# Kernel optimization log

Measured on AMD Instinct MI355X. Metric: run time of the kernel, lower is better.

## Reference

```python
import jax, jax.numpy as jnp
import numpy as np

L, B, H, Y, C = 256, 256, 256, 32, 16  # seq len, batch, hidden, y_size, spline channels (u_size+1)


def setup_inputs() -> dict:
    key = jax.random.key(0)
    ks = jax.random.split(key, 10)
    # times: uniform grid 0..L-1 (torchcde default spline parameterization), shape (L,B,1)
    ts = jnp.broadcast_to(jnp.arange(L, dtype=jnp.float32)[:, None, None], (L, B, 1))
    us = jax.random.normal(ks[0], (L, B, C - 1), dtype=jnp.float32)
    h0 = 0.1 * jax.random.normal(ks[1], (B, H), dtype=jnp.float32)
    s = 1.0 / np.sqrt(H)
    # NCDEFunc: Linear(H,H) -> relu -> Linear(H, H*C) -> tanh -> view(B,H,C)
    W1 = jax.random.uniform(ks[2], (H, H), jnp.float32, -s, s)
    b1 = jax.random.uniform(ks[3], (H,), jnp.float32, -s, s)
    W2 = jax.random.uniform(ks[4], (H, H * C), jnp.float32, -s, s)
    b2 = jax.random.uniform(ks[5], (H * C,), jnp.float32, -s, s)
    # decoder MLP(H, 2H, Y, 1): Linear(H,2H) -> tanh -> Linear(2H,Y)
    dW1 = jax.random.uniform(ks[6], (H, 2 * H), jnp.float32, -s, s)
    db1 = jax.random.uniform(ks[7], (2 * H,), jnp.float32, -s, s)
    s2 = 1.0 / np.sqrt(2 * H)
    dW2 = jax.random.uniform(ks[8], (2 * H, Y), jnp.float32, -s2, s2)
    db2 = jax.random.uniform(ks[9], (Y,), jnp.float32, -s2, s2)
    return dict(ts=ts, us=us, h0=h0, W1=W1, b1=b1, W2=W2, b2=b2,
                dW1=dW1, db1=db1, dW2=dW2, db2=db2)


def reference(ts, us, h0, W1, b1, W2, b2, dW1, db1, dW2, db2):
    # permute to batch-first and build control path x: (B, L, C)
    xb = jnp.concatenate([jnp.transpose(ts, (1, 0, 2)), jnp.transpose(us, (1, 0, 2))], axis=2)
    # hermite cubic with backward differences on unit grid (torchcde default t=arange):
    # node derivative d_i = x_i - x_{i-1} (delta=1); d_0 = d_1
    diffs = xb[:, 1:] - xb[:, :-1]                      # (B, L-1, C)
    dnode = jnp.concatenate([diffs[:, :1], diffs], axis=1)  # (B, L, C)
    t = ts[:, 0, 0]  # (L,) -- cdeint t grid = ts.squeeze(-1)[0,:] after permute

    def dXdt(s_):
        # derivative of the hermite cubic spline at scalar time s_ (unit knot spacing)
        idx = jnp.clip(jnp.floor(s_).astype(jnp.int32), 0, L - 2)
        tau = s_ - idx.astype(s_.dtype)
        xi, xip = xb[:, idx], xb[:, idx + 1]            # (B, C)
        di, dip = dnode[:, idx], dnode[:, idx + 1]
        h00p = 6.0 * tau * tau - 6.0 * tau              # h01' = -h00'
        h10p = 3.0 * tau * tau - 4.0 * tau + 1.0
        h11p = 3.0 * tau * tau - 2.0 * tau
        return h00p * (xi - xip) + h10p * di + h11p * dip  # (B, C)

    def vf(z):
        # NCDEFunc: z (B,H) -> matrix (B,H,C)
        hid = jax.nn.relu(z @ W1 + b1)
        return jnp.tanh(hid @ W2 + b2).reshape(B, H, C)

    def step(z, inp):
        s_, dt_ = inp
        dz = jnp.einsum('bhc,bc->bh', vf(z), dXdt(s_))  # f(z) @ dX/dt
        zn = z + dt_ * dz                               # Euler update on grid t
        return zn, zn

    _, zs = jax.lax.scan(step, h0, (t[:-1], t[1:] - t[:-1]))
    z_seq = jnp.concatenate([h0[None], zs], axis=0)     # (L, B, H): cdeint output at all t
    # decoder then permute(1,0,2) -> already time-major here: (L, B, Y)
    return jnp.tanh(z_seq @ dW1 + db1) @ dW2 + db2
```

## Files before the change

kernel.cpp:

```cpp
#include <hip/hip_runtime.h>
#include <math.h>

#define LL 256
#define BB 256
#define HH 256
#define CC 16
#define YY 32
#define HC (HH*CC)
#define NSTEP (LL-1)
#define NBG 32
#define BGB 8
#define HCH 32
#define TPB 1024
#define NJS 8

typedef __attribute__((ext_vector_type(4))) float f32x4;

__device__ __forceinline__ float fast_tanh(float x) {
    float e = __expf(2.0f * x);
    return 1.0f - 2.0f / (e + 1.0f);
}

__device__ __forceinline__ float ld_coh(const float* p) {
    return __hip_atomic_load(p, __ATOMIC_RELAXED, __HIP_MEMORY_SCOPE_AGENT);
}
__device__ __forceinline__ float2 ld_coh2(const float* p) {
    union { unsigned long long u; float2 f; } cv;
    cv.u = __hip_atomic_load((const unsigned long long*)p,
                             __ATOMIC_RELAXED, __HIP_MEMORY_SCOPE_AGENT);
    return cv.f;
}
__device__ __forceinline__ void st_coh(float* p, float v) {
    __hip_atomic_store(p, v, __ATOMIC_RELAXED, __HIP_MEMORY_SCOPE_AGENT);
}

__device__ __forceinline__ void bg_barrier(unsigned* cnt, unsigned target) {
    __syncthreads();
    if (threadIdx.x == 0) {
        __hip_atomic_fetch_add(cnt, 1u, __ATOMIC_RELAXED, __HIP_MEMORY_SCOPE_AGENT);
        while (__hip_atomic_load(cnt, __ATOMIC_RELAXED, __HIP_MEMORY_SCOPE_AGENT) < target)
            __builtin_amdgcn_s_sleep(1);
    }
    __syncthreads();
}

__global__ void __launch_bounds__(TPB, 4)
k_scan(const float* __restrict__ us, const float* __restrict__ W1,
       const float* __restrict__ b1, const float* __restrict__ W2,
       const float* __restrict__ b2, float* __restrict__ zs,
       float* __restrict__ hidG, unsigned* __restrict__ barG) {
    __shared__ float smem[NJS * BGB * 512 + 2048 + 2048 + 512 + 128 + 32];
    float* psum    = smem;
    float* pa      = smem;
    float* z_loc   = smem + NJS * BGB * 512;
    float* hid_loc = z_loc + BGB * HH;
    float* b2s     = hid_loc + BGB * HH;
    float* dvs     = b2s + 512;
    float* b1s     = dvs + 128;

    const int bg = blockIdx.x >> 3;
    const int hc = blockIdx.x & 7;
    const int t  = threadIdx.x;
    const int b0 = bg * BGB;
    const int h0 = hc * HCH;
    const int n0 = h0 * CC;

    const int ajc = t >> 5;
    const int ah  = t & 31;
    float w1r[8];
    #pragma unroll
    for (int r = 0; r < 8; r++)
        w1r[r] = W1[(size_t)(ajc * 8 + r) * HH + h0 + ah];
    for (int i = t; i < 512; i += TPB) b2s[i] = b2[n0 + i];
    if (t < HCH) b1s[t] = b1[h0 + t];
    __syncthreads();

    unsigned* cnt = barG + (size_t)bg * 64;

    const int sb  = t >> 7;
    const int sj2 = (t & 127) << 1;
    const int jsp = t >> 7;
    const int ct  = (t & 127) << 2;
    const int col = t & 511;
    const int bh  = (t >> 9) << 2;

    for (int k = 0; k < NSTEP; k++) {
        const size_t zk = (size_t)k * (BB * HH);

        {
            float2 v = ld_coh2(&zs[zk + (size_t)(b0 + sb) * HH + sj2]);
            *(float2*)&z_loc[sb * HH + sj2] = v;
        }
        if (t < BGB * CC) {
            int b = t >> 4, c = t & 15;
            int kk = (k < 1) ? 1 : k;
            float v = 1.0f;
            if (c > 0)
                v = us[((size_t)kk * BB + b0 + b) * (CC - 1) + c - 1]
                  - us[((size_t)(kk - 1) * BB + b0 + b) * (CC - 1) + c - 1];
            dvs[b * CC + c] = v;
        }
        __syncthreads();

        {
            float acc[BGB];
            #pragma unroll
            for (int b = 0; b < BGB; b++) acc[b] = 0.f;
            #pragma unroll
            for (int r2 = 0; r2 < 2; r2++) {
                #pragma unroll
                for (int b = 0; b < BGB; b++) {
                    float4 zv = *(const float4*)&z_loc[b * HH + ajc * 8 + r2 * 4];
                    acc[b] += zv.x * w1r[r2 * 4 + 0] + zv.y * w1r[r2 * 4 + 1]
                            + zv.z * w1r[r2 * 4 + 2] + zv.w * w1r[r2 * 4 + 3];
                }
            }
            #pragma unroll
            for (int b = 0; b < BGB; b++)
                pa[ajc * 256 + b * HCH + ah] = acc[b];
        }
        __syncthreads();
        if (t < BGB * HCH) {
            float s = b1s[t & 31];
            #pragma unroll
            for (int q = 0; q < 32; q++) s += pa[q * 256 + t];
            st_coh(&hidG[(size_t)(b0 + (t >> 5)) * HH + h0 + (t & 31)],
                   fmaxf(s, 0.f));
        }
        bg_barrier(cnt, 8u * (2u * (unsigned)k + 1u));

        {
            float2 v = ld_coh2(&hidG[(size_t)(b0 + sb) * HH + sj2]);
            *(float2*)&hid_loc[sb * HH + sj2] = v;
        }
        __syncthreads();

        {
            f32x4 acc[BGB];
            #pragma unroll
            for (int b = 0; b < BGB; b++) acc[b] = (f32x4){0.f, 0.f, 0.f, 0.f};
            const int jb = jsp * 32;
            const float* w2p = &W2[(size_t)jb * HC + n0 + ct];
            #pragma unroll 2
            for (int jq = 0; jq < 32; jq += 4) {
                f32x4 w0 = *(const f32x4*)&w2p[(size_t)(jq + 0) * HC];
                f32x4 w1 = *(const f32x4*)&w2p[(size_t)(jq + 1) * HC];
                f32x4 w2v = *(const f32x4*)&w2p[(size_t)(jq + 2) * HC];
                f32x4 w3 = *(const f32x4*)&w2p[(size_t)(jq + 3) * HC];
                #pragma unroll
                for (int b = 0; b < BGB; b++) {
                    f32x4 h4 = *(const f32x4*)&hid_loc[b * HH + jb + jq];
                    acc[b] = h4.x * w0  + acc[b];
                    acc[b] = h4.y * w1  + acc[b];
                    acc[b] = h4.z * w2v + acc[b];
                    acc[b] = h4.w * w3  + acc[b];
                }
            }
            #pragma unroll
            for (int b = 0; b < BGB; b++)
                *(f32x4*)&psum[((jsp * BGB + b) << 9) + ct] = acc[b];
        }
        __syncthreads();

        {
            #pragma unroll
            for (int q = 0; q < 4; q++) {
                int b = bh + q;
                float g = b2s[col];
                #pragma unroll
                for (int s = 0; s < NJS; s++)
                    g += psum[((s * BGB + b) << 9) + col];
                float v = fast_tanh(g) * dvs[b * CC + (col & 15)];
                v += __shfl_xor(v, 1);
                v += __shfl_xor(v, 2);
                v += __shfl_xor(v, 4);
                v += __shfl_xor(v, 8);
                if ((col & 15) == 0) {
                    int hl = col >> 4;
                    st_coh(&zs[zk + (size_t)(BB * HH) + (size_t)(b0 + b) * HH + h0 + hl],
                           z_loc[b * HH + h0 + hl] + v);
                }
            }
        }
        bg_barrier(cnt, 8u * (2u * (unsigned)k + 2u));
    }
}

__global__ void k_out(const float* __restrict__ zseq, const float* __restrict__ dW1,
                      const float* __restrict__ db1, const float* __restrict__ dW2,
                      const float* __restrict__ db2, float* __restrict__ out) {
    __shared__ float zt[16][HH];
    __shared__ float act[16][2 * HH];
    int r0 = blockIdx.x * 16;
    int t  = threadIdx.x;
    {
        const float4* src = (const float4*)(zseq + (size_t)r0 * HH);
        float4* dst = (float4*)&zt[0][0];
        for (int i = t; i < 1024; i += 256) dst[i] = src[i];
    }
    __syncthreads();
    {
        int c0  = (t & 127) * 4;
        int rr0 = (t >> 7) * 8;
        float a[8][4];
        #pragma unroll
        for (int i = 0; i < 8; i++)
            #pragma unroll
            for (int q = 0; q < 4; q++) a[i][q] = 0.f;
        for (int j = 0; j < HH; j++) {
            float4 w = *(const float4*)&dW1[(size_t)j * 2 * HH + c0];
            #pragma unroll
            for (int i = 0; i < 8; i++) {
                float zv = zt[rr0 + i][j];
                a[i][0] += zv * w.x; a[i][1] += zv * w.y;
                a[i][2] += zv * w.z; a[i][3] += zv * w.w;
            }
        }
        float4 bias = *(const float4*)&db1[c0];
        #pragma unroll
        for (int i = 0; i < 8; i++) {
            act[rr0 + i][c0 + 0] = fast_tanh(a[i][0] + bias.x);
            act[rr0 + i][c0 + 1] = fast_tanh(a[i][1] + bias.y);
            act[rr0 + i][c0 + 2] = fast_tanh(a[i][2] + bias.z);
            act[rr0 + i][c0 + 3] = fast_tanh(a[i][3] + bias.w);
        }
    }
    __syncthreads();
    {
        int rl = t >> 4;
        int y2 = t & 15;
        float o0 = 0.f, o1 = 0.f;
        #pragma unroll 4
        for (int j = 0; j < 2 * HH; j++) {
            float av = act[rl][j];
            float2 w = *(const float2*)&dW2[(size_t)j * YY + y2 * 2];
            o0 += av * w.x; o1 += av * w.y;
        }
        float2 bias = *(const float2*)&db2[y2 * 2];
        out[(size_t)(r0 + rl) * YY + y2 * 2]     = o0 + bias.x;
        out[(size_t)(r0 + rl) * YY + y2 * 2 + 1] = o1 + bias.y;
    }
}

extern "C" void kernel_launch(void* const* d_in, const int* in_sizes, int n_in,
                              void* d_out, int out_size, void* d_ws, size_t ws_size,
                              hipStream_t stream) {
    const float* us  = (const float*)d_in[1];
    const float* h0  = (const float*)d_in[2];
    const float* W1  = (const float*)d_in[3];
    const float* b1  = (const float*)d_in[4];
    const float* W2  = (const float*)d_in[5];
    const float* b2  = (const float*)d_in[6];
    const float* dW1 = (const float*)d_in[7];
    const float* db1 = (const float*)d_in[8];
    const float* dW2 = (const float*)d_in[9];
    const float* db2 = (const float*)d_in[10];
    float* out = (float*)d_out;

    float* zs   = (float*)d_ws;
    float* hidG = zs + (size_t)LL * BB * HH;
    unsigned* barG = (unsigned*)(hidG + (size_t)BB * HH);

    hipMemcpyAsync(zs, h0, (size_t)BB * HH * sizeof(float),
                   hipMemcpyDeviceToDevice, stream);
    hipMemsetAsync(barG, 0, NBG * 64 * sizeof(unsigned), stream);

    k_scan<<<NBG * 8, TPB, 0, stream>>>(us, W1, b1, W2, b2, zs, hidG, barG);
    k_out<<<LL * BB / 16, 256, 0, stream>>>(zs, dW1, db1, dW2, db2, out);
}
```

Measured before the change: 3.513 ms.

## Interleave two batch groups per block with split arrive/wait barriers

Each block now handles two 8-row batch groups (A and B) over a 16-wide hidden slice, instead of one batch group over a 32-wide slice, so 16 blocks cooperate per group pair. The grid barrier is split into separate arrive and wait calls, so one group's compute can overlap the other group's barrier latency. The intent is to hide the cross-block synchronisation cost of the sequential scan. In exchange, each block does less work per phase, W2 is streamed twice per step, and each barrier has more participants (16 instead of 8).

```diff
diff --git a/kernel.cpp b/kernel.cpp
--- a/kernel.cpp
+++ b/kernel.cpp
@@ -10,20 +10,18 @@
 #define NSTEP (LL-1)
 #define NBG 32
 #define BGB 8
-#define HCH 32
+#define NSIB 16
+#define COLS 256
 #define TPB 1024
 #define NJS 8
 
-typedef __attribute__((ext_vector_type(4))) float f32x4;
+typedef __attribute__((ext_vector_type(2))) float f32x2;
 
 __device__ __forceinline__ float fast_tanh(float x) {
     float e = __expf(2.0f * x);
     return 1.0f - 2.0f / (e + 1.0f);
 }
 
-__device__ __forceinline__ float ld_coh(const float* p) {
-    return __hip_atomic_load(p, __ATOMIC_RELAXED, __HIP_MEMORY_SCOPE_AGENT);
-}
 __device__ __forceinline__ float2 ld_coh2(const float* p) {
     union { unsigned long long u; float2 f; } cv;
     cv.u = __hip_atomic_load((const unsigned long long*)p,
@@ -34,13 +32,15 @@
     __hip_atomic_store(p, v, __ATOMIC_RELAXED, __HIP_MEMORY_SCOPE_AGENT);
 }
 
-__device__ __forceinline__ void bg_barrier(unsigned* cnt, unsigned target) {
-    __syncthreads();
-    if (threadIdx.x == 0) {
+__device__ __forceinline__ void bg_arrive(unsigned* cnt) {
+    __syncthreads();
+    if (threadIdx.x == 0)
         __hip_atomic_fetch_add(cnt, 1u, __ATOMIC_RELAXED, __HIP_MEMORY_SCOPE_AGENT);
+}
+__device__ __forceinline__ void bg_wait(unsigned* cnt, unsigned target) {
+    if (threadIdx.x == 0)
         while (__hip_atomic_load(cnt, __ATOMIC_RELAXED, __HIP_MEMORY_SCOPE_AGENT) < target)
             __builtin_amdgcn_s_sleep(1);
-    }
     __syncthreads();
 }
 
@@ -49,140 +49,165 @@
        const float* __restrict__ b1, const float* __restrict__ W2,
        const float* __restrict__ b2, float* __restrict__ zs,
        float* __restrict__ hidG, unsigned* __restrict__ barG) {
-    __shared__ float smem[NJS * BGB * 512 + 2048 + 2048 + 512 + 128 + 32];
-    float* psum    = smem;
-    float* pa      = smem;
-    float* z_loc   = smem + NJS * BGB * 512;
-    float* hid_loc = z_loc + BGB * HH;
-    float* b2s     = hid_loc + BGB * HH;
-    float* dvs     = b2s + 512;
-    float* b1s     = dvs + 128;
-
-    const int bg = blockIdx.x >> 3;
-    const int hc = blockIdx.x & 7;
-    const int t  = threadIdx.x;
-    const int b0 = bg * BGB;
-    const int h0 = hc * HCH;
-    const int n0 = h0 * CC;
-
-    const int ajc = t >> 5;
-    const int ah  = t & 31;
+    __shared__ __align__(16) float smem[23056];
+    float* psum = smem;
+    float* pa   = smem;
+    float* zA   = smem + 16384;
+    float* zB   = zA + 2048;
+    float* hidL = zB + 2048;
+    float* dvsA = hidL + 2048;
+    float* dvsB = dvsA + 128;
+    float* b2s  = dvsB + 128;
+    float* b1s  = b2s + 256;
+
+    const int bp  = blockIdx.x >> 4;
+    const int hc  = (blockIdx.x & 7) * 2 + ((blockIdx.x >> 3) & 1);
+    const int t   = threadIdx.x;
+    const int b0A = (bp * 2) * BGB;
+    const int b0B = (bp * 2 + 1) * BGB;
+    const int h0  = hc * 16;
+    const int n0  = h0 * CC;
+
+    const int ah   = t & 15;
+    const int ajc  = (t >> 4) & 31;
+    const int half = t >> 9;
     float w1r[8];
     #pragma unroll
     for (int r = 0; r < 8; r++)
         w1r[r] = W1[(size_t)(ajc * 8 + r) * HH + h0 + ah];
-    for (int i = t; i < 512; i += TPB) b2s[i] = b2[n0 + i];
-    if (t < HCH) b1s[t] = b1[h0 + t];
-    __syncthreads();
-
-    unsigned* cnt = barG + (size_t)bg * 64;
+    for (int i = t; i < COLS; i += TPB) b2s[i] = b2[n0 + i];
+    if (t < 16) b1s[t] = b1[h0 + t];
+    __syncthreads();
+
+    unsigned* cntA = barG + (size_t)(bp * 2) * 64;
+    unsigned* cntB = barG + (size_t)(bp * 2 + 1) * 64;
 
     const int sb  = t >> 7;
     const int sj2 = (t & 127) << 1;
     const int jsp = t >> 7;
-    const int ct  = (t & 127) << 2;
-    const int col = t & 511;
-    const int bh  = (t >> 9) << 2;
+    const int cp  = (t & 127) << 1;
+    const int col = t & 255;
+    const int bh  = (t >> 8) << 1;
 
     for (int k = 0; k < NSTEP; k++) {
         const size_t zk = (size_t)k * (BB * HH);
 
-        {
-            float2 v = ld_coh2(&zs[zk + (size_t)(b0 + sb) * HH + sj2]);
-            *(float2*)&z_loc[sb * HH + sj2] = v;
-        }
-        if (t < BGB * CC) {
-            int b = t >> 4, c = t & 15;
-            int kk = (k < 1) ? 1 : k;
-            float v = 1.0f;
-            if (c > 0)
-                v = us[((size_t)kk * BB + b0 + b) * (CC - 1) + c - 1]
-                  - us[((size_t)(kk - 1) * BB + b0 + b) * (CC - 1) + c - 1];
-            dvs[b * CC + c] = v;
-        }
-        __syncthreads();
-
-        {
-            float acc[BGB];
-            #pragma unroll
-            for (int b = 0; b < BGB; b++) acc[b] = 0.f;
-            #pragma unroll
-            for (int r2 = 0; r2 < 2; r2++) {
-                #pragma unroll
-                for (int b = 0; b < BGB; b++) {
-                    float4 zv = *(const float4*)&z_loc[b * HH + ajc * 8 + r2 * 4];
-                    acc[b] += zv.x * w1r[r2 * 4 + 0] + zv.y * w1r[r2 * 4 + 1]
-                            + zv.z * w1r[r2 * 4 + 2] + zv.w * w1r[r2 * 4 + 3];
+        #pragma unroll 1
+        for (int pipe = 0; pipe < 2; pipe++) {
+            unsigned* cnt = pipe ? cntB : cntA;
+            float* z_loc  = pipe ? zB : zA;
+            float* dvs    = pipe ? dvsB : dvsA;
+            const int b0  = pipe ? b0B : b0A;
+
+            if (k) bg_wait(cnt, 16u * (2u * (unsigned)k));
+
+            {
+                float2 v = ld_coh2(&zs[zk + (size_t)(b0 + sb) * HH + sj2]);
+                *(float2*)&z_loc[sb * HH + sj2] = v;
+            }
+            if (t < BGB * CC) {
+                int b = t >> 4, c = t & 15;
+                int kk = (k < 1) ? 1 : k;
+                float v = 1.0f;
+                if (c > 0)
+                    v = us[((size_t)kk * BB + b0 + b) * (CC - 1) + c - 1]
+                      - us[((size_t)(kk - 1) * BB + b0 + b) * (CC - 1) + c - 1];
+                dvs[b * CC + c] = v;
+            }
+            __syncthreads();
+
+            {
+                float acc[4];
+                #pragma unroll
+                for (int i = 0; i < 4; i++) acc[i] = 0.f;
+                #pragma unroll
+                for (int r2 = 0; r2 < 2; r2++) {
+                    #pragma unroll
+                    for (int i = 0; i < 4; i++) {
+                        float4 zv = *(const float4*)&z_loc[(half * 4 + i) * HH + ajc * 8 + r2 * 4];
+                        acc[i] += zv.x * w1r[r2 * 4 + 0] + zv.y * w1r[r2 * 4 + 1]
+                                + zv.z * w1r[r2 * 4 + 2] + zv.w * w1r[r2 * 4 + 3];
+                    }
                 }
-            }
-            #pragma unroll
-            for (int b = 0; b < BGB; b++)
-                pa[ajc * 256 + b * HCH + ah] = acc[b];
-        }
-        __syncthreads();
-        if (t < BGB * HCH) {
-            float s = b1s[t & 31];
-            #pragma unroll
-            for (int q = 0; q < 32; q++) s += pa[q * 256 + t];
-            st_coh(&hidG[(size_t)(b0 + (t >> 5)) * HH + h0 + (t & 31)],
-                   fmaxf(s, 0.f));
-        }
-        bg_barrier(cnt, 8u * (2u * (unsigned)k + 1u));
-
-        {
-            float2 v = ld_coh2(&hidG[(size_t)(b0 + sb) * HH + sj2]);
-            *(float2*)&hid_loc[sb * HH + sj2] = v;
-        }
-        __syncthreads();
-
-        {
-            f32x4 acc[BGB];
-            #pragma unroll
-            for (int b = 0; b < BGB; b++) acc[b] = (f32x4){0.f, 0.f, 0.f, 0.f};
-            const int jb = jsp * 32;
-            const float* w2p = &W2[(size_t)jb * HC + n0 + ct];
-            #pragma unroll 2
-            for (int jq = 0; jq < 32; jq += 4) {
-                f32x4 w0 = *(const f32x4*)&w2p[(size_t)(jq + 0) * HC];
-                f32x4 w1 = *(const f32x4*)&w2p[(size_t)(jq + 1) * HC];
-                f32x4 w2v = *(const f32x4*)&w2p[(size_t)(jq + 2) * HC];
-                f32x4 w3 = *(const f32x4*)&w2p[(size_t)(jq + 3) * HC];
-                #pragma unroll
-                for (int b = 0; b < BGB; b++) {
-                    f32x4 h4 = *(const f32x4*)&hid_loc[b * HH + jb + jq];
-                    acc[b] = h4.x * w0  + acc[b];
-                    acc[b] = h4.y * w1  + acc[b];
-                    acc[b] = h4.z * w2v + acc[b];
-                    acc[b] = h4.w * w3  + acc[b];
+                #pragma unroll
+                for (int i = 0; i < 4; i++)
+                    pa[ajc * 132 + (half * 4 + i) * 16 + ah] = acc[i];
+            }
+            __syncthreads();
+            if (t < BGB * 16) {
+                float s = b1s[t & 15];
+                #pragma unroll
+                for (int q = 0; q < 32; q++) s += pa[q * 132 + t];
+                st_coh(&hidG[(size_t)(b0 + (t >> 4)) * HH + h0 + (t & 15)],
+                       fmaxf(s, 0.f));
+            }
+            bg_arrive(cnt);
+        }
+
+        #pragma unroll 1
+        for (int pipe = 0; pipe < 2; pipe++) {
+            unsigned* cnt = pipe ? cntB : cntA;
+            float* z_loc  = pipe ? zB : zA;
+            float* dvs    = pipe ? dvsB : dvsA;
+            const int b0  = pipe ? b0B : b0A;
+
+            bg_wait(cnt, 16u * (2u * (unsigned)k + 1u));
+
+            {
+                float2 v = ld_coh2(&hidG[(size_t)(b0 + sb) * HH + sj2]);
+                *(float2*)&hidL[sb * HH + sj2] = v;
+            }
+            __syncthreads();
+
+            {
+                f32x2 acc[BGB];
+                #pragma unroll
+                for (int b = 0; b < BGB; b++) acc[b] = (f32x2){0.f, 0.f};
+                const int jb = jsp * 32;
+                const float* w2p = &W2[(size_t)jb * HC + n0 + cp];
+                #pragma unroll 2
+                for (int jq = 0; jq < 32; jq += 4) {
+                    f32x2 w0 = *(const f32x2*)&w2p[(size_t)(jq + 0) * HC];
+                    f32x2 w1 = *(const f32x2*)&w2p[(size_t)(jq + 1) * HC];
+                    f32x2 w2v = *(const f32x2*)&w2p[(size_t)(jq + 2) * HC];
+                    f32x2 w3 = *(const f32x2*)&w2p[(size_t)(jq + 3) * HC];
+                    #pragma unroll
+                    for (int b = 0; b < BGB; b++) {
+                        float4 h4 = *(const float4*)&hidL[b * HH + jb + jq];
+                        acc[b] = h4.x * w0  + acc[b];
+                        acc[b] = h4.y * w1  + acc[b];
+                        acc[b] = h4.z * w2v + acc[b];
+                        acc[b] = h4.w * w3  + acc[b];
+                    }
                 }
-            }
-            #pragma unroll
-            for (int b = 0; b < BGB; b++)
-                *(f32x4*)&psum[((jsp * BGB + b) << 9) + ct] = acc[b];
-        }
-        __syncthreads();
-
-        {
-            #pragma unroll
-            for (int q = 0; q < 4; q++) {
-                int b = bh + q;
-                float g = b2s[col];
-                #pragma unroll
-                for (int s = 0; s < NJS; s++)
-                    g += psum[((s * BGB + b) << 9) + col];
-                float v = fast_tanh(g) * dvs[b * CC + (col & 15)];
-                v += __shfl_xor(v, 1);
-                v += __shfl_xor(v, 2);
-                v += __shfl_xor(v, 4);
-                v += __shfl_xor(v, 8);
-                if ((col & 15) == 0) {
-                    int hl = col >> 4;
-                    st_coh(&zs[zk + (size_t)(BB * HH) + (size_t)(b0 + b) * HH + h0 + hl],
-                           z_loc[b * HH + h0 + hl] + v);
+                #pragma unroll
+                for (int b = 0; b < BGB; b++)
+                    *(f32x2*)&psum[((jsp * BGB + b) << 8) + cp] = acc[b];
+            }
+            __syncthreads();
+
+            {
+                #pragma unroll
+                for (int q = 0; q < 2; q++) {
+                    int b = bh + q;
+                    float g = b2s[col];
+                    #pragma unroll
+                    for (int s = 0; s < NJS; s++)
+                        g += psum[((s * BGB + b) << 8) + col];
+                    float v = fast_tanh(g) * dvs[b * CC + (col & 15)];
+                    v += __shfl_xor(v, 1);
+                    v += __shfl_xor(v, 2);
+                    v += __shfl_xor(v, 4);
+                    v += __shfl_xor(v, 8);
+                    if ((col & 15) == 0) {
+                        int hl = col >> 4;
+                        st_coh(&zs[zk + (size_t)(BB * HH) + (size_t)(b0 + b) * HH + h0 + hl],
+                               z_loc[b * HH + h0 + hl] + v);
+                    }
                 }
             }
-        }
-        bg_barrier(cnt, 8u * (2u * (unsigned)k + 2u));
+            bg_arrive(cnt);
+        }
     }
 }
 
@@ -265,6 +290,6 @@
                    hipMemcpyDeviceToDevice, stream);
     hipMemsetAsync(barG, 0, NBG * 64 * sizeof(unsigned), stream);
 
-    k_scan<<<NBG * 8, TPB, 0, stream>>>(us, W1, b1, W2, b2, zs, hidG, barG);
+    k_scan<<<256, TPB, 0, stream>>>(us, W1, b1, W2, b2, zs, hidG, barG);
     k_out<<<LL * BB / 16, 256, 0, stream>>>(zs, dW1, db1, dW2, db2, out);
 }
```

New measurement: 4.612 ms. 31.3% more time.
